# Kernel optimization log

Measured on AMD Instinct MI355X. Metric: run time of the kernel, lower is better.

The kernel has to match this reference:

```python
import jax, jax.numpy as jnp
import numpy as np

B, A, D = 256, 128, 5          # batch, max_atoms, max_degree
FA, FB, C = 256, 64, 256       # atom feats, bond feats, conv_width


def setup_inputs() -> dict:
    key = jax.random.key(0)
    k1, k2, k3, k4 = jax.random.split(key, 4)
    atoms = jax.random.normal(k1, (B, A, FA), dtype=jnp.float32)
    bonds = jax.random.normal(k2, (B, A, D, FB), dtype=jnp.float32)
    # neighbour indices with -1 as padding value
    edges = jax.random.randint(k3, (B, A, D), -1, A, dtype=jnp.int32)
    W = jax.random.normal(k4, (D, FA + FB, C), dtype=jnp.float32) * 0.05
    b = jnp.zeros((D, C), dtype=jnp.float32)
    return {"atoms": atoms, "bonds": bonds, "edges": edges, "W": W, "b": b}


def reference(atoms, bonds, edges, W, b):
    # atom degree = number of non-padding neighbours  (B, A)
    deg = jnp.sum(edges != -1, axis=-1)

    # neighbour_lookup: pad a zero atom at index 0, shift indices by +1 so -1 -> 0
    masked_atoms = jnp.pad(atoms, ((0, 0), (1, 0), (0, 0)))        # (B, A+1, FA)
    idx = edges + 1                                                # (B, A, D)
    neigh = masked_atoms[jnp.arange(B)[:, None, None], idx]        # (B, A, D, FA)

    # include_self=True then sum over neighbour axis == self + sum(neighbours)
    summed_atom = atoms + jnp.sum(neigh, axis=2)                   # (B, A, FA)
    summed_bond = jnp.sum(bonds, axis=2)                           # (B, A, FB)
    feat = jnp.concatenate([summed_atom, summed_bond], axis=-1)    # (B, A, FA+FB)

    # per-degree Dense (relu), masked by (degree == d), summed over degrees
    dense = jax.nn.relu(jnp.einsum('baf,dfc->badc', feat, W) + b)  # (B, A, D, C)
    mask = (deg[..., None] == jnp.arange(D)).astype(dense.dtype)   # (B, A, D)
    return jnp.einsum('badc,bad->bac', dense, mask)                # (B, A, C)
```

## Files before the change

### kernel.cpp

```cpp
#include <hip/hip_runtime.h>


#define NB 256
#define NA 128
#define ND 5
#define NFA 256
#define NFB 64
#define NC 256
#define NF (NFA + NFB)

__global__ __launch_bounds__(256) void ngh_kernel(
    const float* __restrict__ atoms,
    const float* __restrict__ bonds,
    const int*   __restrict__ edges,
    const float* __restrict__ W,
    const float* __restrict__ bias,
    float* __restrict__ out)
{
    const int row = blockIdx.x;
    const int b   = row >> 7;
    const int a   = row & (NA - 1);
    const int t   = threadIdx.x;

    int e[ND];
    int deg = 0;
#pragma unroll
    for (int d = 0; d < ND; ++d) {
        e[d] = edges[row * ND + d];
        deg += (e[d] != -1) ? 1 : 0;
    }

    float* orow = out + (size_t)row * NC;

    if (deg >= ND) {
        orow[t] = 0.0f;
        return;
    }

    __shared__ float feat[NF];
    {
        const float* arow = atoms + ((size_t)b * NA + a) * NFA;
        float v = arow[t];
#pragma unroll
        for (int d = 0; d < ND; ++d) {
            if (e[d] != -1) {
                v += atoms[((size_t)b * NA + e[d]) * NFA + t];
            }
        }
        feat[t] = v;
    }
    if (t < NFB) {
        const float* brow = bonds + ((size_t)b * NA + a) * (ND * NFB);
        float v = 0.0f;
#pragma unroll
        for (int d = 0; d < ND; ++d) v += brow[d * NFB + t];
        feat[NFA + t] = v;
    }
    __syncthreads();

    const float* Wd = W + (size_t)deg * NF * NC + t;
    float acc = bias[deg * NC + t];
#pragma unroll 8
    for (int f = 0; f < NF; ++f) {
        acc = fmaf(feat[f], Wd[(size_t)f * NC], acc);
    }
    orow[t] = fmaxf(acc, 0.0f);
}

extern "C" void kernel_launch(void* const* d_in, const int* in_sizes, int n_in,
                              void* d_out, int out_size, void* d_ws, size_t ws_size,
                              hipStream_t stream) {
    const float* atoms = (const float*)d_in[0];
    const float* bonds = (const float*)d_in[1];
    const int*   edges = (const int*)  d_in[2];
    const float* W     = (const float*)d_in[3];
    const float* bias  = (const float*)d_in[4];
    float*       out   = (float*)d_out;

    dim3 grid(NB * NA);
    dim3 block(NC);
    ngh_kernel<<<grid, block, 0, stream>>>(atoms, bonds, edges, W, bias, out);
}
```

Before: 134.6 us.

## Bucket rows by degree and batch eight rows per weight pass

A first kernel zeroes the output and sorts rows into per-degree lists using atomic counters. A persistent second kernel then processes groups of eight rows that share a degree, so each weight column load is reused across eight rows instead of one. This cuts W traffic roughly eightfold, but adds a memset, an extra kernel launch, atomics, and a grid of only 256 blocks, which may limit occupancy.

Result: slower. 153.4 us (+14.0%).

```diff
diff --git a/kernel.cpp b/kernel.cpp
--- a/kernel.cpp
+++ b/kernel.cpp
@@ -7,64 +7,117 @@
 #define NFA 256
 #define NFB 64
 #define NC 256
-#define NF (NFA + NFB)
+#define NF 320
+#define NROWS (NB * NA)
+#define GROUP 8
 
-__global__ __launch_bounds__(256) void ngh_kernel(
+__global__ __launch_bounds__(256) void classify_zero(
+    const int* __restrict__ edges,
+    float4* __restrict__ out4,
+    int* __restrict__ cnt,
+    int* __restrict__ lists)
+{
+    const int tid = blockIdx.x * 256 + threadIdx.x;
+    const int total4 = NROWS * NC / 4;
+    for (int i = tid; i < total4; i += 256 * 256)
+        out4[i] = make_float4(0.f, 0.f, 0.f, 0.f);
+
+    if (tid < NROWS) {
+        int deg = 0;
+#pragma unroll
+        for (int d = 0; d < ND; ++d)
+            deg += (edges[tid * ND + d] != -1) ? 1 : 0;
+        if (deg < ND) {
+            int idx = atomicAdd(&cnt[deg], 1);
+            lists[deg * NROWS + idx] = tid;
+        }
+    }
+}
+
+__global__ __launch_bounds__(256) void matvec(
     const float* __restrict__ atoms,
     const float* __restrict__ bonds,
     const int*   __restrict__ edges,
     const float* __restrict__ W,
     const float* __restrict__ bias,
+    const int*   __restrict__ cnt,
+    const int*   __restrict__ lists,
     float* __restrict__ out)
 {
-    const int row = blockIdx.x;
-    const int b   = row >> 7;
-    const int a   = row & (NA - 1);
-    const int t   = threadIdx.x;
+    __shared__ int   rows_s[GROUP];
+    __shared__ float feat[GROUP][NF];
 
-    int e[ND];
-    int deg = 0;
+    const int t = threadIdx.x;
+
+    int pre[ND + 1];
+    pre[0] = 0;
 #pragma unroll
-    for (int d = 0; d < ND; ++d) {
-        e[d] = edges[row * ND + d];
-        deg += (e[d] != -1) ? 1 : 0;
-    }
+    for (int d = 0; d < ND; ++d)
+        pre[d + 1] = pre[d] + (cnt[d] + GROUP - 1) / GROUP;
+    const int total_tiles = pre[ND];
 
-    float* orow = out + (size_t)row * NC;
+    for (int tile = blockIdx.x; tile < total_tiles; tile += gridDim.x) {
+        int d = 0;
+        while (tile >= pre[d + 1]) ++d;
+        const int base = (tile - pre[d]) * GROUP;
+        const int n = min(GROUP, cnt[d] - base);
 
-    if (deg >= ND) {
-        orow[t] = 0.0f;
-        return;
-    }
+        __syncthreads();
+        if (t < GROUP)
+            rows_s[t] = (t < n) ? lists[d * NROWS + base + t] : -1;
+        __syncthreads();
 
-    __shared__ float feat[NF];
-    {
-        const float* arow = atoms + ((size_t)b * NA + a) * NFA;
-        float v = arow[t];
 #pragma unroll
-        for (int d = 0; d < ND; ++d) {
-            if (e[d] != -1) {
-                v += atoms[((size_t)b * NA + e[d]) * NFA + t];
+        for (int r = 0; r < GROUP; ++r) {
+            const int row = rows_s[r];
+            if (row < 0) continue;
+            const int b = row >> 7;
+            float v = atoms[(size_t)row * NFA + t];
+#pragma unroll
+            for (int dd = 0; dd < ND; ++dd) {
+                const int e = edges[row * ND + dd];
+                if (e != -1)
+                    v += atoms[((size_t)(b * NA + e)) * NFA + t];
+            }
+            feat[r][t] = v;
+            if (t < NFB) {
+                float s = 0.f;
+#pragma unroll
+                for (int dd = 0; dd < ND; ++dd)
+                    s += bonds[(size_t)row * (ND * NFB) + dd * NFB + t];
+                feat[r][NFA + t] = s;
             }
         }
-        feat[t] = v;
+        __syncthreads();
+
+        float acc[GROUP];
+        const float bv = bias[d * NC + t];
+#pragma unroll
+        for (int r = 0; r < GROUP; ++r) acc[r] = bv;
+
+        const float* Wd = W + (size_t)d * NF * NC + t;
+        for (int f = 0; f < NF; f += 4) {
+            const float w0 = Wd[(size_t)(f + 0) * NC];
+            const float w1 = Wd[(size_t)(f + 1) * NC];
+            const float w2 = Wd[(size_t)(f + 2) * NC];
+            const float w3 = Wd[(size_t)(f + 3) * NC];
+#pragma unroll
+            for (int r = 0; r < GROUP; ++r) {
+                const float4 fe = *(const float4*)&feat[r][f];
+                acc[r] = fmaf(fe.x, w0,
+                         fmaf(fe.y, w1,
+                         fmaf(fe.z, w2,
+                         fmaf(fe.w, w3, acc[r]))));
+            }
+        }
+
+#pragma unroll
+        for (int r = 0; r < GROUP; ++r) {
+            const int row = rows_s[r];
+            if (row >= 0)
+                out[(size_t)row * NC + t] = fmaxf(acc[r], 0.f);
+        }
     }
-    if (t < NFB) {
-        const float* brow = bonds + ((size_t)b * NA + a) * (ND * NFB);
-        float v = 0.0f;
-#pragma unroll
-        for (int d = 0; d < ND; ++d) v += brow[d * NFB + t];
-        feat[NFA + t] = v;
-    }
-    __syncthreads();
-
-    const float* Wd = W + (size_t)deg * NF * NC + t;
-    float acc = bias[deg * NC + t];
-#pragma unroll 8
-    for (int f = 0; f < NF; ++f) {
-        acc = fmaf(feat[f], Wd[(size_t)f * NC], acc);
-    }
-    orow[t] = fmaxf(acc, 0.0f);
 }
 
 extern "C" void kernel_launch(void* const* d_in, const int* in_sizes, int n_in,
@@ -77,7 +130,10 @@
     const float* bias  = (const float*)d_in[4];
     float*       out   = (float*)d_out;
 
-    dim3 grid(NB * NA);
-    dim3 block(NC);
-    ngh_kernel<<<grid, block, 0, stream>>>(atoms, bonds, edges, W, bias, out);
+    int* cnt   = (int*)d_ws;
+    int* lists = (int*)d_ws + 8;
+
+    hipMemsetAsync(cnt, 0, 8 * sizeof(int), stream);
+    classify_zero<<<256, 256, 0, stream>>>(edges, (float4*)out, cnt, lists);
+    matvec<<<256, 256, 0, stream>>>(atoms, bonds, edges, W, bias, cnt, lists, out);
 }
```

## Process one molecule per block, bucketing atoms by degree for weight reuse

Applied to the files above, without the earlier changes.

Replaces the one-block-per-atom kernel with one block per molecule. Atoms are bucketed by degree in shared memory and processed in groups of up to 8. Each wavefront computes two rows with float4 weight loads, so each weight load is reused across several atoms instead of once per atom. The grid shrinks to 256 blocks with launch_bounds(256,1) and many serial syncs, so parallelism and latency hiding drop sharply.

Measured after the change: 142.6 us. 6.0% more time.

```diff
diff --git a/kernel.cpp b/kernel.cpp
--- a/kernel.cpp
+++ b/kernel.cpp
@@ -1,15 +1,15 @@
 #include <hip/hip_runtime.h>
 
 
-#define NB 256
+#define ND 5
 #define NA 128
-#define ND 5
 #define NFA 256
 #define NFB 64
 #define NC 256
-#define NF (NFA + NFB)
+#define NF 320
+#define GROUP 8
 
-__global__ __launch_bounds__(256) void ngh_kernel(
+__global__ __launch_bounds__(256, 1) void ngh_fused(
     const float* __restrict__ atoms,
     const float* __restrict__ bonds,
     const int*   __restrict__ edges,
@@ -17,54 +17,122 @@
     const float* __restrict__ bias,
     float* __restrict__ out)
 {
-    const int row = blockIdx.x;
-    const int b   = row >> 7;
-    const int a   = row & (NA - 1);
-    const int t   = threadIdx.x;
+    const int b    = blockIdx.x;
+    const int t    = threadIdx.x;
+    const int lane = t & 63;
+    const int wv   = t >> 6;
 
-    int e[ND];
-    int deg = 0;
+    __shared__ int   edges_s[NA * ND];
+    __shared__ int   deg_s[NA];
+    __shared__ int   hlist[ND][NA];
+    __shared__ int   hcnt[ND];
+    __shared__ float feat[GROUP][NF];
+
+    if (t < ND) hcnt[t] = 0;
+    for (int i = t; i < NA * ND; i += 256)
+        edges_s[i] = edges[b * (NA * ND) + i];
+    __syncthreads();
+
+    if (t < NA) {
+        int deg = 0;
 #pragma unroll
-    for (int d = 0; d < ND; ++d) {
-        e[d] = edges[row * ND + d];
-        deg += (e[d] != -1) ? 1 : 0;
-    }
-
-    float* orow = out + (size_t)row * NC;
-
-    if (deg >= ND) {
-        orow[t] = 0.0f;
-        return;
-    }
-
-    __shared__ float feat[NF];
-    {
-        const float* arow = atoms + ((size_t)b * NA + a) * NFA;
-        float v = arow[t];
-#pragma unroll
-        for (int d = 0; d < ND; ++d) {
-            if (e[d] != -1) {
-                v += atoms[((size_t)b * NA + e[d]) * NFA + t];
-            }
+        for (int dd = 0; dd < ND; ++dd)
+            deg += (edges_s[t * ND + dd] != -1) ? 1 : 0;
+        deg_s[t] = deg;
+        if (deg < ND) {
+            int idx = atomicAdd(&hcnt[deg], 1);
+            hlist[deg][idx] = t;
         }
-        feat[t] = v;
-    }
-    if (t < NFB) {
-        const float* brow = bonds + ((size_t)b * NA + a) * (ND * NFB);
-        float v = 0.0f;
-#pragma unroll
-        for (int d = 0; d < ND; ++d) v += brow[d * NFB + t];
-        feat[NFA + t] = v;
     }
     __syncthreads();
 
-    const float* Wd = W + (size_t)deg * NF * NC + t;
-    float acc = bias[deg * NC + t];
-#pragma unroll 8
-    for (int f = 0; f < NF; ++f) {
-        acc = fmaf(feat[f], Wd[(size_t)f * NC], acc);
+    {
+        float4* out4 = (float4*)out + (size_t)b * (NA * NC / 4);
+        for (int i = t; i < NA * NC / 4; i += 256) {
+            if (deg_s[i >> 6] == ND)
+                out4[i] = make_float4(0.f, 0.f, 0.f, 0.f);
+        }
     }
-    orow[t] = fmaxf(acc, 0.0f);
+
+    for (int d = 0; d < ND; ++d) {
+        const int nd = hcnt[d];
+        const float4* W4 = (const float4*)W + (size_t)d * (NF * NC / 4) + lane;
+        for (int base = 0; base < nd; base += GROUP) {
+            const int n = min(GROUP, nd - base);
+            __syncthreads();
+            for (int r = 0; r < n; ++r) {
+                const int rl  = hlist[d][base + r];
+                const int row = b * NA + rl;
+                float v = atoms[(size_t)row * NFA + t];
+#pragma unroll
+                for (int dd = 0; dd < ND; ++dd) {
+                    const int e = edges_s[rl * ND + dd];
+                    if (e >= 0)
+                        v += atoms[(size_t)(b * NA + e) * NFA + t];
+                }
+                feat[r][t] = v;
+                if (t < NFB) {
+                    float s = 0.f;
+#pragma unroll
+                    for (int dd = 0; dd < ND; ++dd)
+                        s += bonds[((size_t)row * ND + dd) * NFB + t];
+                    feat[r][NFA + t] = s;
+                }
+            }
+            __syncthreads();
+
+            const int r0 = wv, r1 = wv + 4;
+            const float4 bv = ((const float4*)bias)[d * (NC / 4) + lane];
+            float4* out4 = (float4*)out + (size_t)b * (NA * NC / 4) + lane;
+
+            if (r1 < n) {
+                const float4* f0 = (const float4*)feat[r0];
+                const float4* f1 = (const float4*)feat[r1];
+                float4 a0 = bv, a1 = bv;
+#pragma unroll 4
+                for (int fc = 0; fc < NF / 4; ++fc) {
+                    const float4 e0 = f0[fc];
+                    const float4 e1 = f1[fc];
+#pragma unroll
+                    for (int j = 0; j < 4; ++j) {
+                        const float4 w = W4[(fc * 4 + j) * (NC / 4)];
+                        const float s0 = j == 0 ? e0.x : j == 1 ? e0.y : j == 2 ? e0.z : e0.w;
+                        const float s1 = j == 0 ? e1.x : j == 1 ? e1.y : j == 2 ? e1.z : e1.w;
+                        a0.x = fmaf(s0, w.x, a0.x); a0.y = fmaf(s0, w.y, a0.y);
+                        a0.z = fmaf(s0, w.z, a0.z); a0.w = fmaf(s0, w.w, a0.w);
+                        a1.x = fmaf(s1, w.x, a1.x); a1.y = fmaf(s1, w.y, a1.y);
+                        a1.z = fmaf(s1, w.z, a1.z); a1.w = fmaf(s1, w.w, a1.w);
+                    }
+                }
+                const int rowl0 = hlist[d][base + r0];
+                const int rowl1 = hlist[d][base + r1];
+                out4[(size_t)rowl0 * (NC / 4)] =
+                    make_float4(fmaxf(a0.x, 0.f), fmaxf(a0.y, 0.f),
+                                fmaxf(a0.z, 0.f), fmaxf(a0.w, 0.f));
+                out4[(size_t)rowl1 * (NC / 4)] =
+                    make_float4(fmaxf(a1.x, 0.f), fmaxf(a1.y, 0.f),
+                                fmaxf(a1.z, 0.f), fmaxf(a1.w, 0.f));
+            } else if (r0 < n) {
+                const float4* f0 = (const float4*)feat[r0];
+                float4 a0 = bv;
+#pragma unroll 4
+                for (int fc = 0; fc < NF / 4; ++fc) {
+                    const float4 e0 = f0[fc];
+#pragma unroll
+                    for (int j = 0; j < 4; ++j) {
+                        const float4 w = W4[(fc * 4 + j) * (NC / 4)];
+                        const float s0 = j == 0 ? e0.x : j == 1 ? e0.y : j == 2 ? e0.z : e0.w;
+                        a0.x = fmaf(s0, w.x, a0.x); a0.y = fmaf(s0, w.y, a0.y);
+                        a0.z = fmaf(s0, w.z, a0.z); a0.w = fmaf(s0, w.w, a0.w);
+                    }
+                }
+                const int rowl0 = hlist[d][base + r0];
+                out4[(size_t)rowl0 * (NC / 4)] =
+                    make_float4(fmaxf(a0.x, 0.f), fmaxf(a0.y, 0.f),
+                                fmaxf(a0.z, 0.f), fmaxf(a0.w, 0.f));
+            }
+        }
+    }
 }
 
 extern "C" void kernel_launch(void* const* d_in, const int* in_sizes, int n_in,
@@ -77,7 +145,5 @@
     const float* bias  = (const float*)d_in[4];
     float*       out   = (float*)d_out;
 
-    dim3 grid(NB * NA);
-    dim3 block(NC);
-    ngh_kernel<<<grid, block, 0, stream>>>(atoms, bonds, edges, W, bias, out);
+    ngh_fused<<<256, 256, 0, stream>>>(atoms, bonds, edges, W, bias, out);
 }
```

## Process 16 rows per block with one wavefront per row and readlane broadcasts

Applied to the files above, without the earlier changes.

The kernel moves from one block per atom row to blocks of 16 rows, giving each wavefront a whole row. Each lane keeps gathered features in registers and broadcasts them with readlane, so the shared-memory feature staging and per-row sync go away. Each lane computes four output channels with float4 weight loads, and rows with full degree are zeroed with vectorized stores. Rows are split round-robin across the four wavefronts, which can leave wavefronts unevenly loaded, and there are fewer blocks in flight.

Measured after the change: 137.5 us. 1.02x slower.

```diff
diff --git a/kernel.cpp b/kernel.cpp
--- a/kernel.cpp
+++ b/kernel.cpp
@@ -1,13 +1,18 @@
 #include <hip/hip_runtime.h>
 
 
-#define NB 256
+#define ND 5
 #define NA 128
-#define ND 5
 #define NFA 256
 #define NFB 64
 #define NC 256
-#define NF (NFA + NFB)
+#define NF 320
+#define RPB 16
+#define NBLK 2048
+
+__device__ __forceinline__ float bcast(float v, int l) {
+    return __int_as_float(__builtin_amdgcn_readlane(__float_as_int(v), l));
+}
 
 __global__ __launch_bounds__(256) void ngh_kernel(
     const float* __restrict__ atoms,
@@ -17,54 +22,95 @@
     const float* __restrict__ bias,
     float* __restrict__ out)
 {
-    const int row = blockIdx.x;
-    const int b   = row >> 7;
-    const int a   = row & (NA - 1);
-    const int t   = threadIdx.x;
+    const int t     = threadIdx.x;
+    const int lane  = t & 63;
+    const int wv    = t >> 6;
+    const int rbase = blockIdx.x * RPB;
 
-    int e[ND];
-    int deg = 0;
+    __shared__ int edges_s[RPB * ND];
+    __shared__ int deg_s[RPB];
+
+    if (t < RPB * ND) edges_s[t] = edges[rbase * ND + t];
+    __syncthreads();
+
+    if (t < RPB) {
+        int deg = 0;
 #pragma unroll
-    for (int d = 0; d < ND; ++d) {
-        e[d] = edges[row * ND + d];
-        deg += (e[d] != -1) ? 1 : 0;
-    }
-
-    float* orow = out + (size_t)row * NC;
-
-    if (deg >= ND) {
-        orow[t] = 0.0f;
-        return;
-    }
-
-    __shared__ float feat[NF];
-    {
-        const float* arow = atoms + ((size_t)b * NA + a) * NFA;
-        float v = arow[t];
-#pragma unroll
-        for (int d = 0; d < ND; ++d) {
-            if (e[d] != -1) {
-                v += atoms[((size_t)b * NA + e[d]) * NFA + t];
-            }
-        }
-        feat[t] = v;
-    }
-    if (t < NFB) {
-        const float* brow = bonds + ((size_t)b * NA + a) * (ND * NFB);
-        float v = 0.0f;
-#pragma unroll
-        for (int d = 0; d < ND; ++d) v += brow[d * NFB + t];
-        feat[NFA + t] = v;
+        for (int dd = 0; dd < ND; ++dd)
+            deg += (edges_s[t * ND + dd] != -1) ? 1 : 0;
+        deg_s[t] = deg;
     }
     __syncthreads();
 
-    const float* Wd = W + (size_t)deg * NF * NC + t;
-    float acc = bias[deg * NC + t];
-#pragma unroll 8
-    for (int f = 0; f < NF; ++f) {
-        acc = fmaf(feat[f], Wd[(size_t)f * NC], acc);
+    {
+        float4* out4 = (float4*)out + (size_t)rbase * (NC / 4);
+#pragma unroll
+        for (int k = 0; k < RPB * (NC / 4) / 256; ++k) {
+            const int i = t + 256 * k;
+            if (deg_s[i >> 6] == ND)
+                out4[i] = make_float4(0.f, 0.f, 0.f, 0.f);
+        }
     }
-    orow[t] = fmaxf(acc, 0.0f);
+
+    int h = 0;
+    for (int rl = 0; rl < RPB; ++rl) {
+        const int d = deg_s[rl];
+        if (d >= ND) continue;
+        if ((h++ & 3) != wv) continue;
+
+        const int row = rbase + rl;
+        const int bb  = row >> 7;
+
+        const int e0 = edges_s[rl * ND + 0];
+        const int e1 = edges_s[rl * ND + 1];
+        const int e2 = edges_s[rl * ND + 2];
+        const int e3 = edges_s[rl * ND + 3];
+        const int e4 = edges_s[rl * ND + 4];
+
+        const float* arow = atoms + (size_t)row * NFA;
+        float f0 = arow[      lane];
+        float f1 = arow[ 64 + lane];
+        float f2 = arow[128 + lane];
+        float f3 = arow[192 + lane];
+#define ADD_NEIGH(E)                                                       \
+        if ((E) >= 0) {                                                    \
+            const float* nr = atoms + (size_t)(bb * NA + (E)) * NFA;       \
+            f0 += nr[      lane];                                          \
+            f1 += nr[ 64 + lane];                                          \
+            f2 += nr[128 + lane];                                          \
+            f3 += nr[192 + lane];                                          \
+        }
+        ADD_NEIGH(e0) ADD_NEIGH(e1) ADD_NEIGH(e2) ADD_NEIGH(e3) ADD_NEIGH(e4)
+#undef ADD_NEIGH
+        float fb = 0.f;
+#pragma unroll
+        for (int dd = 0; dd < ND; ++dd)
+            fb += bonds[((size_t)row * ND + dd) * NFB + lane];
+
+        const float4* W4 = (const float4*)W + (size_t)d * NF * (NC / 4) + lane;
+        float4 acc = ((const float4*)bias)[d * (NC / 4) + lane];
+
+#define FMA_CHUNK(FREG, FBASE)                                             \
+        _Pragma("unroll 16")                                               \
+        for (int l = 0; l < 64; ++l) {                                     \
+            const float  s = bcast((FREG), l);                             \
+            const float4 w = W4[(size_t)((FBASE) + l) * (NC / 4)];         \
+            acc.x = fmaf(s, w.x, acc.x);                                   \
+            acc.y = fmaf(s, w.y, acc.y);                                   \
+            acc.z = fmaf(s, w.z, acc.z);                                   \
+            acc.w = fmaf(s, w.w, acc.w);                                   \
+        }
+        FMA_CHUNK(f0,   0)
+        FMA_CHUNK(f1,  64)
+        FMA_CHUNK(f2, 128)
+        FMA_CHUNK(f3, 192)
+        FMA_CHUNK(fb, 256)
+#undef FMA_CHUNK
+
+        ((float4*)out)[(size_t)row * (NC / 4) + lane] =
+            make_float4(fmaxf(acc.x, 0.f), fmaxf(acc.y, 0.f),
+                        fmaxf(acc.z, 0.f), fmaxf(acc.w, 0.f));
+    }
 }
 
 extern "C" void kernel_launch(void* const* d_in, const int* in_sizes, int n_in,
@@ -77,7 +123,5 @@
     const float* bias  = (const float*)d_in[4];
     float*       out   = (float*)d_out;
 
-    dim3 grid(NB * NA);
-    dim3 block(NC);
-    ngh_kernel<<<grid, block, 0, stream>>>(atoms, bonds, edges, W, bias, out);
+    ngh_kernel<<<NBLK, 256, 0, stream>>>(atoms, bonds, edges, W, bias, out);
 }
```
